# Kernel tuning notes

Hardware: AMD Instinct MI355X
Metric: run time of the kernel (lower is better)

Reference implementation:

```python
import jax, jax.numpy as jnp
import numpy as np


def _image_to_patches(x, fh, fw):
    # x: [N, H, W, C] -> [N, num_patches, fh, fw, C] (non-overlapping patches)
    N, H, W, C = x.shape
    nr, nc = H // fh, W // fw
    x = x.reshape(N, nr, fh, nc, fw, C)
    x = x.transpose(0, 1, 3, 2, 4, 5)  # [N, nr, nc, fh, fw, C]
    return x.reshape(N, nr * nc, fh, fw, C)


def setup_inputs() -> dict:
    key = jax.random.key(0)
    k1, k2 = jax.random.split(key, 2)
    N, H, W, FIN = 64, 128, 128, 32
    FH, FW, FOUT = 8, 8, 128
    P = (H // FH) * (W // FW)  # 256 patches
    X = jax.random.normal(k1, (N, H, W, FIN), dtype=jnp.float32)
    # 'alexnet' init: normal(0, 0.01); leading broadcast dim of 1 dropped
    filters = jax.random.normal(k2, (P, FH, FW, FIN, FOUT), dtype=jnp.float32) * 0.01
    bias = jnp.zeros((FOUT,), dtype=jnp.float32)  # tf.ones(fout) * 0.0
    return {"X": X, "filters": filters, "bias": bias}


def reference(X, filters, bias):
    N, H, W, C = X.shape
    P, FH, FW, FIN, FOUT = filters.shape
    nr, nc = H // FH, W // FW
    patches = _image_to_patches(X, FH, FW)  # [N, P, FH, FW, FIN]
    # Original: broadcast-multiply [N,P,fh,fw,fin,1] * [1,P,fh,fw,fin,fout],
    # reduce over (fh, fw, fin). Same math as a per-patch (unshared) GEMM:
    Z = jnp.einsum('npijc,pijco->npo', patches, filters)  # [N, P, FOUT]
    Z = Z + bias  # broadcast over [N, P]
    Z = Z.reshape(N, nr, nc, FOUT)
    return jax.nn.relu(Z)
```

## Files before the change

kernel.cpp:

```cpp
#include <hip/hip_runtime.h>
#include <hip/hip_bf16.h>

typedef __attribute__((ext_vector_type(8))) __bf16 bf16x8;
typedef __attribute__((ext_vector_type(8))) short  short8;
typedef __attribute__((ext_vector_type(4))) float  f32x4;

#define NIMG   64
#define FOUTC  128
#define KTOT   2048
#define BK     64
#define NSTEP  32

#define A_HI   0
#define A_LO   8192
#define B_HI   16384
#define B_LO   32768
#define BUFSZ  49152

__device__ __forceinline__ int addrA(int row, int slot) {
  return row * 128 + (((slot ^ row) & 7) << 4);
}
__device__ __forceinline__ int addrB(int o, int slot) {
  return o * 128 + (((slot ^ o) & 7) << 4);
}

__device__ __forceinline__ void cvt2(float f, short& h, short& l) {
  __hip_bfloat16 bh = __float2bfloat16(f);
  float fh = __bfloat162float(bh);
  __hip_bfloat16 bl = __float2bfloat16(f - fh);
  h = (short)__builtin_bit_cast(unsigned short, bh);
  l = (short)__builtin_bit_cast(unsigned short, bl);
}

struct StageRegs {
  float4 a0, a1;
  float  b[16];
};

__device__ __forceinline__ void issue_loads(const float* __restrict__ X,
                                            const float* __restrict__ F,
                                            int kb, int t, int p, int r, int c,
                                            StageRegs& R) {
  const int n = t >> 3, slot = t & 7;
  const int arow = r * 32768 + (kb >> 2) * 4096 + c * 256 + (kb & 3) * 64;
  const float* ap = X + n * 524288 + arow + slot * 8;
  R.a0 = *(const float4*)(ap);
  R.a1 = *(const float4*)(ap + 4);
  const int o = t & 127, sg = t >> 7;
  const float* bp = F + p * 262144 + kb * 8192 + o;
#pragma unroll
  for (int h = 0; h < 2; ++h) {
    const int ks = sg + h * 4;
#pragma unroll
    for (int j = 0; j < 8; ++j)
      R.b[h * 8 + j] = bp[(ks * 8 + j) * 128];
  }
}

__device__ __forceinline__ void stage_write(char* buf, int t, const StageRegs& R) {
  const int n = t >> 3, slot = t & 7;
  float av[8];
  av[0] = R.a0.x; av[1] = R.a0.y; av[2] = R.a0.z; av[3] = R.a0.w;
  av[4] = R.a1.x; av[5] = R.a1.y; av[6] = R.a1.z; av[7] = R.a1.w;
  short8 h, l;
#pragma unroll
  for (int e = 0; e < 8; ++e) { short hh, ll; cvt2(av[e], hh, ll); h[e] = hh; l[e] = ll; }
  const int aoff = addrA(n, slot);
  *(short8*)(buf + A_HI + aoff) = h;
  *(short8*)(buf + A_LO + aoff) = l;

  const int o = t & 127, sg = t >> 7;
#pragma unroll
  for (int hh2 = 0; hh2 < 2; ++hh2) {
    const int ks = sg + hh2 * 4;
    short8 bh, bl;
#pragma unroll
    for (int j = 0; j < 8; ++j) { short x, y; cvt2(R.b[hh2 * 8 + j], x, y); bh[j] = x; bl[j] = y; }
    const int boff = addrB(o, ks);
    *(short8*)(buf + B_HI + boff) = bh;
    *(short8*)(buf + B_LO + boff) = bl;
  }
}

__device__ __forceinline__ void mfma_step(const char* buf, int wm, int wn, int lane,
                                          f32x4 acc[4]) {
  const int arow = wm * 16 + (lane & 15);
  const int grp = lane >> 4;
#pragma unroll
  for (int ks = 0; ks < 2; ++ks) {
    const int slot = grp + ks * 4;
    const int aoff = addrA(arow, slot);
    bf16x8 ah = *(const bf16x8*)(buf + A_HI + aoff);
    bf16x8 al = *(const bf16x8*)(buf + A_LO + aoff);
#pragma unroll
    for (int nf = 0; nf < 4; ++nf) {
      const int o = wn * 64 + nf * 16 + (lane & 15);
      const int boff = addrB(o, slot);
      bf16x8 bh = *(const bf16x8*)(buf + B_HI + boff);
      bf16x8 bl = *(const bf16x8*)(buf + B_LO + boff);
      acc[nf] = __builtin_amdgcn_mfma_f32_16x16x32_bf16(ah, bh, acc[nf], 0, 0, 0);
      acc[nf] = __builtin_amdgcn_mfma_f32_16x16x32_bf16(ah, bl, acc[nf], 0, 0, 0);
      acc[nf] = __builtin_amdgcn_mfma_f32_16x16x32_bf16(al, bh, acc[nf], 0, 0, 0);
    }
  }
}

__global__ __launch_bounds__(512, 2)
void bioconv_kernel(const float* __restrict__ X, const float* __restrict__ F,
                    const float* __restrict__ bias, float* __restrict__ out) {
  __shared__ __align__(16) char lds[2 * BUFSZ];
  const int p = blockIdx.x;
  const int r = p >> 4, c = p & 15;
  const int t = threadIdx.x;
  const int lane = t & 63;
  const int w = t >> 6;
  const int wm = w & 3;
  const int wn = w >> 2;

  f32x4 acc[4] = {f32x4{0,0,0,0}, f32x4{0,0,0,0}, f32x4{0,0,0,0}, f32x4{0,0,0,0}};

  StageRegs Ra, Rb;
  issue_loads(X, F, 0, t, p, r, c, Ra);
  stage_write(lds, t, Ra);
  issue_loads(X, F, 1, t, p, r, c, Rb);
  __syncthreads();

  for (int kb = 0; kb < NSTEP; kb += 2) {
    mfma_step(lds, wm, wn, lane, acc);
    if (kb + 2 < NSTEP) issue_loads(X, F, kb + 2, t, p, r, c, Ra);
    stage_write(lds + BUFSZ, t, Rb);
    __syncthreads();
    mfma_step(lds + BUFSZ, wm, wn, lane, acc);
    if (kb + 3 < NSTEP) issue_loads(X, F, kb + 3, t, p, r, c, Rb);
    if (kb + 2 < NSTEP) stage_write(lds, t, Ra);
    __syncthreads();
  }

  const int colb = wn * 64 + (lane & 15);
  const int rowb = wm * 16 + (lane >> 4) * 4;
#pragma unroll
  for (int nf = 0; nf < 4; ++nf) {
    const int col = colb + nf * 16;
    const float bv = bias[col];
#pragma unroll
    for (int j = 0; j < 4; ++j) {
      float v = acc[nf][j] + bv;
      v = fmaxf(v, 0.0f);
      out[(rowb + j) * 32768 + p * 128 + col] = v;
    }
  }
}

extern "C" void kernel_launch(void* const* d_in, const int* in_sizes, int n_in,
                              void* d_out, int out_size, void* d_ws, size_t ws_size,
                              hipStream_t stream) {
  const float* X    = (const float*)d_in[0];
  const float* F    = (const float*)d_in[1];
  const float* bias = (const float*)d_in[2];
  float* out = (float*)d_out;
  hipLaunchKernelGGL(bioconv_kernel, dim3(256), dim3(512), 0, stream, X, F, bias, out);
}
```

Before: 432.2 us.

## Split output channels across two blocks per patch to double grid size

Each patch's GEMM is now split into two blocks, each covering 64 of the 128 output channels, so the grid grows from 256 to 512 blocks. Per-block LDS drops from 96KB to 64KB, the B staging registers are halved, and launch bounds request 4 blocks per SM. This targets poor occupancy and underfilled CUs on a 256-CU device with only 256 blocks. The cost is that the X tile for each patch is now loaded and split into bf16 hi/lo twice, once per half.

```diff
diff --git a/kernel.cpp b/kernel.cpp
--- a/kernel.cpp
+++ b/kernel.cpp
@@ -5,17 +5,13 @@
 typedef __attribute__((ext_vector_type(8))) short  short8;
 typedef __attribute__((ext_vector_type(4))) float  f32x4;
 
-#define NIMG   64
-#define FOUTC  128
-#define KTOT   2048
-#define BK     64
 #define NSTEP  32
 
 #define A_HI   0
 #define A_LO   8192
 #define B_HI   16384
-#define B_LO   32768
-#define BUFSZ  49152
+#define B_LO   24576
+#define BUFSZ  32768
 
 __device__ __forceinline__ int addrA(int row, int slot) {
   return row * 128 + (((slot ^ row) & 7) << 4);
@@ -34,27 +30,23 @@
 
 struct StageRegs {
   float4 a0, a1;
-  float  b[16];
+  float  b[8];
 };
 
 __device__ __forceinline__ void issue_loads(const float* __restrict__ X,
                                             const float* __restrict__ F,
                                             int kb, int t, int p, int r, int c,
-                                            StageRegs& R) {
+                                            int og, StageRegs& R) {
   const int n = t >> 3, slot = t & 7;
   const int arow = r * 32768 + (kb >> 2) * 4096 + c * 256 + (kb & 3) * 64;
   const float* ap = X + n * 524288 + arow + slot * 8;
   R.a0 = *(const float4*)(ap);
   R.a1 = *(const float4*)(ap + 4);
-  const int o = t & 127, sg = t >> 7;
-  const float* bp = F + p * 262144 + kb * 8192 + o;
+  const int o = t & 63, sg = t >> 6;
+  const float* bp = F + p * 262144 + kb * 8192 + og + o;
 #pragma unroll
-  for (int h = 0; h < 2; ++h) {
-    const int ks = sg + h * 4;
-#pragma unroll
-    for (int j = 0; j < 8; ++j)
-      R.b[h * 8 + j] = bp[(ks * 8 + j) * 128];
-  }
+  for (int e = 0; e < 8; ++e)
+    R.b[e] = bp[(sg * 8 + e) * 128];
 }
 
 __device__ __forceinline__ void stage_write(char* buf, int t, const StageRegs& R) {
@@ -69,21 +61,17 @@
   *(short8*)(buf + A_HI + aoff) = h;
   *(short8*)(buf + A_LO + aoff) = l;
 
-  const int o = t & 127, sg = t >> 7;
+  const int o = t & 63, sg = t >> 6;
+  short8 bh, bl;
 #pragma unroll
-  for (int hh2 = 0; hh2 < 2; ++hh2) {
-    const int ks = sg + hh2 * 4;
-    short8 bh, bl;
-#pragma unroll
-    for (int j = 0; j < 8; ++j) { short x, y; cvt2(R.b[hh2 * 8 + j], x, y); bh[j] = x; bl[j] = y; }
-    const int boff = addrB(o, ks);
-    *(short8*)(buf + B_HI + boff) = bh;
-    *(short8*)(buf + B_LO + boff) = bl;
-  }
+  for (int e = 0; e < 8; ++e) { short x, y; cvt2(R.b[e], x, y); bh[e] = x; bl[e] = y; }
+  const int boff = addrB(o, sg);
+  *(short8*)(buf + B_HI + boff) = bh;
+  *(short8*)(buf + B_LO + boff) = bl;
 }
 
 __device__ __forceinline__ void mfma_step(const char* buf, int wm, int wn, int lane,
-                                          f32x4 acc[4]) {
+                                          f32x4 acc[2]) {
   const int arow = wm * 16 + (lane & 15);
   const int grp = lane >> 4;
 #pragma unroll
@@ -93,8 +81,8 @@
     bf16x8 ah = *(const bf16x8*)(buf + A_HI + aoff);
     bf16x8 al = *(const bf16x8*)(buf + A_LO + aoff);
 #pragma unroll
-    for (int nf = 0; nf < 4; ++nf) {
-      const int o = wn * 64 + nf * 16 + (lane & 15);
+    for (int nf = 0; nf < 2; ++nf) {
+      const int o = wn * 32 + nf * 16 + (lane & 15);
       const int boff = addrB(o, slot);
       bf16x8 bh = *(const bf16x8*)(buf + B_HI + boff);
       bf16x8 bl = *(const bf16x8*)(buf + B_LO + boff);
@@ -105,11 +93,13 @@
   }
 }
 
-__global__ __launch_bounds__(512, 2)
+__global__ __launch_bounds__(512, 4)
 void bioconv_kernel(const float* __restrict__ X, const float* __restrict__ F,
                     const float* __restrict__ bias, float* __restrict__ out) {
   __shared__ __align__(16) char lds[2 * BUFSZ];
-  const int p = blockIdx.x;
+  const int s = blockIdx.x >> 8;
+  const int p = blockIdx.x & 255;
+  const int og = s * 64;
   const int r = p >> 4, c = p & 15;
   const int t = threadIdx.x;
   const int lane = t & 63;
@@ -117,29 +107,29 @@
   const int wm = w & 3;
   const int wn = w >> 2;
 
-  f32x4 acc[4] = {f32x4{0,0,0,0}, f32x4{0,0,0,0}, f32x4{0,0,0,0}, f32x4{0,0,0,0}};
+  f32x4 acc[2] = {f32x4{0,0,0,0}, f32x4{0,0,0,0}};
 
   StageRegs Ra, Rb;
-  issue_loads(X, F, 0, t, p, r, c, Ra);
+  issue_loads(X, F, 0, t, p, r, c, og, Ra);
   stage_write(lds, t, Ra);
-  issue_loads(X, F, 1, t, p, r, c, Rb);
+  issue_loads(X, F, 1, t, p, r, c, og, Rb);
   __syncthreads();
 
   for (int kb = 0; kb < NSTEP; kb += 2) {
     mfma_step(lds, wm, wn, lane, acc);
-    if (kb + 2 < NSTEP) issue_loads(X, F, kb + 2, t, p, r, c, Ra);
+    if (kb + 2 < NSTEP) issue_loads(X, F, kb + 2, t, p, r, c, og, Ra);
     stage_write(lds + BUFSZ, t, Rb);
     __syncthreads();
     mfma_step(lds + BUFSZ, wm, wn, lane, acc);
-    if (kb + 3 < NSTEP) issue_loads(X, F, kb + 3, t, p, r, c, Rb);
+    if (kb + 3 < NSTEP) issue_loads(X, F, kb + 3, t, p, r, c, og, Rb);
     if (kb + 2 < NSTEP) stage_write(lds, t, Ra);
     __syncthreads();
   }
 
-  const int colb = wn * 64 + (lane & 15);
+  const int colb = og + wn * 32 + (lane & 15);
   const int rowb = wm * 16 + (lane >> 4) * 4;
 #pragma unroll
-  for (int nf = 0; nf < 4; ++nf) {
+  for (int nf = 0; nf < 2; ++nf) {
     const int col = colb + nf * 16;
     const float bv = bias[col];
 #pragma unroll
@@ -158,5 +148,5 @@
   const float* F    = (const float*)d_in[1];
   const float* bias = (const float*)d_in[2];
   float* out = (float*)d_out;
-  hipLaunchKernelGGL(bioconv_kernel, dim3(256), dim3(512), 0, stream, X, F, bias, out);
+  hipLaunchKernelGGL(bioconv_kernel, dim3(512), dim3(512), 0, stream, X, F, bias, out);
 }
```

After: 443.1 us. 2.5% more time.
